# Kernel optimization log

Hardware: AMD Instinct MI355X
Metric: run time of the kernel (lower is better)

The kernel has to match this reference:

```python
import jax, jax.numpy as jnp
import numpy as np

N = 10000        # nodes
E = 320000       # edges (before self-loops)
G = 100          # graphs in batch
HEADS = 2
OUT = 125        # per-head out channels
NEG_SLOPE = 0.2  # PyG GATConv default leaky_relu slope


def setup_inputs() -> dict:
    key = jax.random.key(0)
    k = lambda i: jax.random.fold_in(key, i)
    rn = lambda i, shape, s=0.1: jax.random.normal(k(i), shape, jnp.float32) * s
    inp = {
        "x": jax.random.normal(k(0), (N, 336), jnp.float32),
        "edge_index": jax.random.randint(k(1), (2, E), 0, N, jnp.int32),
        "batch": jnp.sort(jax.random.randint(k(2), (N,), 0, G, jnp.int32)),
    }
    conv_in = [336, 250, 250, 250]
    for i, din in enumerate(conv_in, start=1):
        base = 10 * i
        inp[f"W{i}"] = rn(base, (din, HEADS * OUT))
        inp[f"asrc{i}"] = rn(base + 1, (HEADS, OUT))
        inp[f"adst{i}"] = rn(base + 2, (HEADS, OUT))
        inp[f"b{i}"] = jnp.zeros((HEADS * OUT,), jnp.float32)
    lin_dims = [(250, 200), (200, 100), (100, 100), (100, 29)]
    for i, (din, dout) in enumerate(lin_dims, start=1):
        inp[f"lw{i}"] = rn(100 + i, (din, dout))
        inp[f"lb{i}"] = jnp.zeros((dout,), jnp.float32)
    return inp


def gat_conv(x, src, dst, W, asrc, adst, b):
    # PyG GATConv (v1), concat heads, self-loops already in (src, dst).
    n = x.shape[0]
    h = (x @ W).reshape(n, HEADS, OUT)                    # [N,H,C]
    e_src = jnp.einsum('nhc,hc->nh', h, asrc)             # a_src . h_j
    e_dst = jnp.einsum('nhc,hc->nh', h, adst)             # a_dst . h_i
    e = jax.nn.leaky_relu(e_src[src] + e_dst[dst], NEG_SLOPE)  # [Etot,H]
    m = jax.ops.segment_max(e, dst, num_segments=n)       # segment softmax over incoming edges
    e = jnp.exp(e - m[dst])
    denom = jax.ops.segment_sum(e, dst, num_segments=n)
    alpha = e / (denom[dst] + 1e-16)                      # [Etot,H]
    out = jax.ops.segment_sum(alpha[:, :, None] * h[src], dst, num_segments=n)
    return out.reshape(n, HEADS * OUT) + b


def reference(x, edge_index, batch,
              W1, asrc1, adst1, b1, W2, asrc2, adst2, b2,
              W3, asrc3, adst3, b3, W4, asrc4, adst4, b4,
              lw1, lb1, lw2, lb2, lw3, lb3, lw4, lb4):
    n = x.shape[0]
    loop = jnp.arange(n, dtype=edge_index.dtype)
    src = jnp.concatenate([edge_index[0], loop])          # add_self_loops=True
    dst = jnp.concatenate([edge_index[1], loop])

    h = jax.nn.relu(gat_conv(x, src, dst, W1, asrc1, adst1, b1))
    h = jax.nn.relu(gat_conv(h, src, dst, W2, asrc2, adst2, b2))
    h = jax.nn.relu(gat_conv(h, src, dst, W3, asrc3, adst3, b3))
    h = jax.nn.relu(gat_conv(h, src, dst, W4, asrc4, adst4, b4))

    # global_mean_pool over graph ids
    sums = jax.ops.segment_sum(h, batch, num_segments=G)
    cnts = jax.ops.segment_sum(jnp.ones((n, 1), h.dtype), batch, num_segments=G)
    g = sums / jnp.maximum(cnts, 1.0)                     # [G,250]

    g = jax.nn.relu(g @ lw1 + lb1)
    g = jax.nn.relu(g @ lw2 + lb2)
    g = jax.nn.relu(g @ lw3 + lb3)
    return g @ lw4 + lb4                                  # [G,29]
```

## Files before the change

kernel.cpp:

```cpp
#include <hip/hip_runtime.h>
#include <hip/hip_bf16.h>

#define NNODES 10000
#define NEDGES 320000
#define ETOT   (NEDGES + NNODES)
#define NGRAPH 100
#define CH     250
#define HOUT   125
#define MPAD   10048
#define KP0    352
#define KP1    256
#define HPAD   256
#define DCAP   256

typedef __attribute__((ext_vector_type(8))) short bf16x8;
typedef __attribute__((ext_vector_type(4))) float f32x4;

static __device__ __forceinline__ float bfbits2f(unsigned int u){
  union{ unsigned int i; float f; } v; v.i = u << 16; return v.f;
}
static __device__ __forceinline__ unsigned short f2bfbits(float f){
  __hip_bfloat16 b = __float2bfloat16(f);
  union{ __hip_bfloat16 b; unsigned short s; } v; v.b = b; return v.s;
}

__global__ void k_deg(const int* __restrict__ eidx, int* __restrict__ deg,
                      const int* __restrict__ batch, int* __restrict__ gstart){
  int e = blockIdx.x*blockDim.x + threadIdx.x;
  if (e < ETOT){
    int dst = (e < NEDGES) ? eidx[NEDGES + e] : (e - NEDGES);
    atomicAdd(&deg[dst], 1);
  }
  if (e < NNODES){
    int b1 = batch[e];
    int b0 = (e == 0) ? -1 : batch[e-1];
    for (int b = b0 + 1; b <= b1; ++b) gstart[b] = e;
    if (e == NNODES - 1){
      for (int b = b1 + 1; b <= NGRAPH; ++b) gstart[b] = NNODES;
    }
  }
}

__global__ __launch_bounds__(1024) void k_scan(const int* __restrict__ deg, int* __restrict__ rowptr){
  const int CHUNK = 10;
  int tid = threadIdx.x;
  int base = tid * CHUNK;
  int sum = 0;
  #pragma unroll
  for (int u = 0; u < CHUNK; ++u){
    int i = base + u;
    sum += (i < NNODES) ? deg[i] : 0;
  }
  int lane = tid & 63, wv = tid >> 6;
  int v = sum;
  #pragma unroll
  for (int off = 1; off < 64; off <<= 1){
    int t = __shfl_up(v, off);
    if (lane >= off) v += t;
  }
  __shared__ int wtot[16];
  __shared__ int woff[16];
  if (lane == 63) wtot[wv] = v;
  __syncthreads();
  if (tid == 0){
    int acc = 0;
    #pragma unroll
    for (int w = 0; w < 16; ++w){ woff[w] = acc; acc += wtot[w]; }
  }
  __syncthreads();
  int run = woff[wv] + v - sum;
  #pragma unroll
  for (int u = 0; u < CHUNK; ++u){
    int i = base + u;
    if (i < NNODES){
      run += deg[i];
      rowptr[i+1] = run;
    }
  }
  if (tid == 0) rowptr[0] = 0;
}

__global__ void k_fill(const int* __restrict__ eidx, const int* __restrict__ rowptr,
                       int* __restrict__ cursor, int* __restrict__ csr_src){
  int e = blockIdx.x*blockDim.x + threadIdx.x;
  if (e >= ETOT) return;
  int dst, src;
  if (e < NEDGES){ src = eidx[e]; dst = eidx[NEDGES + e]; }
  else           { src = e - NEDGES; dst = src; }
  int pos = atomicAdd(&cursor[dst], 1);
  csr_src[rowptr[dst] + pos] = src;
}

__global__ void k_xconv(const float* __restrict__ x, __hip_bfloat16* __restrict__ Ab){
  int idx = blockIdx.x*blockDim.x + threadIdx.x;
  if (idx >= NNODES*336) return;
  int r = idx / 336, k = idx % 336;
  Ab[(size_t)r * KP0 + k] = __float2bfloat16(x[idx]);
}

__global__ void k_wconv_all(const float* __restrict__ W0, const float* __restrict__ W1,
                            const float* __restrict__ W2, const float* __restrict__ W3,
                            __hip_bfloat16* __restrict__ Wt0, __hip_bfloat16* __restrict__ Wt1,
                            __hip_bfloat16* __restrict__ Wt2, __hip_bfloat16* __restrict__ Wt3){
  const int T0 = 16 * KP0 * 16;
  const int T1 = 16 * KP1 * 16;
  int idx = blockIdx.x*blockDim.x + threadIdx.x;
  const float* W; __hip_bfloat16* Wt; int K, Kp, li;
  if (idx < T0)              { W = W0; Wt = Wt0; K = 336; Kp = KP0; li = idx; }
  else if (idx < T0 +   T1)  { W = W1; Wt = Wt1; K = CH;  Kp = KP1; li = idx - T0; }
  else if (idx < T0 + 2*T1)  { W = W2; Wt = Wt2; K = CH;  Kp = KP1; li = idx - T0 - T1; }
  else if (idx < T0 + 3*T1)  { W = W3; Wt = Wt3; K = CH;  Kp = KP1; li = idx - T0 - 2*T1; }
  else return;
  int KC = Kp >> 5;
  int nt = li / (Kp * 16);
  int rem = li % (Kp * 16);
  int k = rem / 16;
  int n = rem % 16;
  int col = nt * 16 + n;
  float v = (k < K && col < CH) ? W[(size_t)k * CH + col] : 0.f;
  Wt[(((size_t)nt * KC + (k >> 5)) * 16 + n) * 32 + (k & 31)] = __float2bfloat16(v);
}

__global__ __launch_bounds__(256) void k_gemm_mfma(
    const __hip_bfloat16* __restrict__ A, const __hip_bfloat16* __restrict__ Wt,
    __hip_bfloat16* __restrict__ Cb, const float* __restrict__ asrc,
    const float* __restrict__ adst, float* __restrict__ esrc, float* __restrict__ edst,
    int M, int Kp){
  int wv = threadIdx.x >> 6, lane = threadIdx.x & 63;
  int n16 = lane & 15, q = lane >> 4;
  int KC = Kp >> 5;
  int rowbase = blockIdx.x * 64 + wv * 16;
  int bn = blockIdx.y * 64;
  int nt0 = bn >> 4;
  const __hip_bfloat16* ap = A  + (size_t)(rowbase + n16) * Kp + q * 8;
  const __hip_bfloat16* bp = Wt + ((size_t)nt0 * KC * 16 + n16) * 32 + q * 8;
  f32x4 ac0 = {0.f,0.f,0.f,0.f}, ac1 = ac0, ac2 = ac0, ac3 = ac0;
  for (int kc = 0; kc < KC; ++kc){
    bf16x8 a  = *(const bf16x8*)(ap + (size_t)kc * 32);
    bf16x8 b0 = *(const bf16x8*)(bp + ((size_t)0 * KC + kc) * 512);
    bf16x8 b1 = *(const bf16x8*)(bp + ((size_t)1 * KC + kc) * 512);
    bf16x8 b2 = *(const bf16x8*)(bp + ((size_t)2 * KC + kc) * 512);
    bf16x8 b3 = *(const bf16x8*)(bp + ((size_t)3 * KC + kc) * 512);
    ac0 = __builtin_amdgcn_mfma_f32_16x16x32_bf16(a, b0, ac0, 0, 0, 0);
    ac1 = __builtin_amdgcn_mfma_f32_16x16x32_bf16(a, b1, ac1, 0, 0, 0);
    ac2 = __builtin_amdgcn_mfma_f32_16x16x32_bf16(a, b2, ac2, 0, 0, 0);
    ac3 = __builtin_amdgcn_mfma_f32_16x16x32_bf16(a, b3, ac3, 0, 0, 0);
  }
  float es0[4] = {}, es1[4] = {}, ed0a[4] = {}, ed1a[4] = {};
  #define SCORE_T(AC, T) { \
    int col = bn + (T)*16 + n16; \
    bool ok = col < CH; \
    float av = ok ? asrc[col] : 0.f; \
    float dv = ok ? adst[col] : 0.f; \
    bool hh = col >= HOUT; \
    float av0 = hh ? 0.f : av, av1 = hh ? av : 0.f; \
    float dv0 = hh ? 0.f : dv, dv1 = hh ? dv : 0.f; \
    _Pragma("unroll") \
    for (int r = 0; r < 4; ++r){ \
      es0[r] += AC[r]*av0; es1[r] += AC[r]*av1; \
      ed0a[r] += AC[r]*dv0; ed1a[r] += AC[r]*dv1; } }
  SCORE_T(ac0, 0) SCORE_T(ac1, 1) SCORE_T(ac2, 2) SCORE_T(ac3, 3)
  #undef SCORE_T
  #pragma unroll
  for (int off = 1; off < 16; off <<= 1){
    #pragma unroll
    for (int r = 0; r < 4; ++r){
      es0[r]  += __shfl_xor(es0[r],  off);
      es1[r]  += __shfl_xor(es1[r],  off);
      ed0a[r] += __shfl_xor(ed0a[r], off);
      ed1a[r] += __shfl_xor(ed1a[r], off);
    }
  }
  if (n16 == 0){
    #pragma unroll
    for (int r = 0; r < 4; ++r){
      int row = rowbase + q*4 + r;
      if (row < M){
        atomicAdd(&esrc[row*2+0], es0[r]);
        atomicAdd(&esrc[row*2+1], es1[r]);
        atomicAdd(&edst[row*2+0], ed0a[r]);
        atomicAdd(&edst[row*2+1], ed1a[r]);
      }
    }
  }
  #pragma unroll
  for (int r = 0; r < 4; ++r){
    int row = rowbase + q * 4 + r;
    if (row >= M) continue;
    int col = bn + n16;
    __hip_bfloat16* cb = Cb + (size_t)row * HPAD + col;
    if (col      < CH) cb[0]  = __float2bfloat16(ac0[r]);
    if (col + 16 < CH) cb[16] = __float2bfloat16(ac1[r]);
    if (col + 32 < CH) cb[32] = __float2bfloat16(ac2[r]);
    if (col + 48 < CH) cb[48] = __float2bfloat16(ac3[r]);
  }
}

__global__ __launch_bounds__(256) void k_attn(const __hip_bfloat16* __restrict__ h,
                        const float* __restrict__ esrc, const float* __restrict__ edst,
                        const int* __restrict__ rowptr, const int* __restrict__ csr_src,
                        const float* __restrict__ bias, __hip_bfloat16* __restrict__ outb,
                        float* __restrict__ esZ, float* __restrict__ edZ){
  int node = blockIdx.x;
  int tid = threadIdx.x, wave = tid >> 6, lane = tid & 63;
  int start = rowptr[node], deg = rowptr[node+1] - start;
  __shared__ int   s_src[DCAP];
  __shared__ float s_x0[DCAP], s_x1[DCAP];
  __shared__ float wred0[4], wred1[4];
  __shared__ float sh[4 * 256];
  float ed0 = edst[node*2+0], ed1 = edst[node*2+1];
  float sm0 = 0.f, sm1 = 0.f;
  for (int i = tid; i < deg; i += 256){
    int src = csr_src[start + i];
    float e0 = esrc[src*2+0] + ed0; e0 = e0 > 0.f ? e0 : 0.2f*e0;
    float e1 = esrc[src*2+1] + ed1; e1 = e1 > 0.f ? e1 : 0.2f*e1;
    float x0 = __expf(e0), x1 = __expf(e1);
    if (i < DCAP){ s_src[i] = src; s_x0[i] = x0; s_x1[i] = x1; }
    sm0 += x0; sm1 += x1;
  }
  for (int off = 32; off > 0; off >>= 1){
    sm0 += __shfl_xor(sm0, off);
    sm1 += __shfl_xor(sm1, off);
  }
  if (lane == 0){ wred0[wave] = sm0; wred1[wave] = sm1; }
  __syncthreads();
  float inv0 = 1.f / ((wred0[0]+wred0[1]+wred0[2]+wred0[3]) + 1e-16f);
  float inv1 = 1.f / ((wred1[0]+wred1[1]+wred1[2]+wred1[3]) + 1e-16f);
  int c0 = 4*lane;
  bool h0_0 = (c0    ) < HOUT, h0_1 = (c0 + 1) < HOUT;
  bool h0_2 = (c0 + 2) < HOUT, h0_3 = (c0 + 3) < HOUT;
  float acc0=0.f, acc1=0.f, acc2=0.f, acc3=0.f;
  #define FETCH(I, S, A0, A1) { \
    if ((I) < DCAP){ S = s_src[I]; A0 = s_x0[I]*inv0; A1 = s_x1[I]*inv1; } \
    else { S = csr_src[start + (I)]; \
      float e0 = esrc[S*2+0] + ed0; e0 = e0 > 0.f ? e0 : 0.2f*e0; \
      float e1 = esrc[S*2+1] + ed1; e1 = e1 > 0.f ? e1 : 0.2f*e1; \
      A0 = __expf(e0)*inv0; A1 = __expf(e1)*inv1; } }
  #define GATHER(S, A0, A1) { \
    uint2 d = *(const uint2*)(h + (size_t)(S) * HPAD + c0); \
    acc0 += (h0_0 ? A0 : A1) * bfbits2f(d.x & 0xffffu); \
    acc1 += (h0_1 ? A0 : A1) * bfbits2f(d.x >> 16); \
    acc2 += (h0_2 ? A0 : A1) * bfbits2f(d.y & 0xffffu); \
    acc3 += (h0_3 ? A0 : A1) * bfbits2f(d.y >> 16); }
  int i = wave;
  for (; i + 4 < deg; i += 8){
    int sA, sB; float a0A,a1A,a0B,a1B;
    FETCH(i, sA, a0A, a1A)
    FETCH(i+4, sB, a0B, a1B)
    GATHER(sA, a0A, a1A)
    GATHER(sB, a0B, a1B)
  }
  if (i < deg){
    int sA; float a0A, a1A;
    FETCH(i, sA, a0A, a1A)
    GATHER(sA, a0A, a1A)
  }
  #undef GATHER
  #undef FETCH
  float* shw = sh + wave * 256;
  *(float4*)&shw[c0] = make_float4(acc0, acc1, acc2, acc3);
  __syncthreads();
  if (tid < 62){
    int c = 4*tid;
    float4 b4 = *(const float4*)&bias[c];
    float v0 = sh[c]   + sh[256+c]   + sh[512+c]   + sh[768+c]   + b4.x;
    float v1 = sh[c+1] + sh[256+c+1] + sh[512+c+1] + sh[768+c+1] + b4.y;
    float v2 = sh[c+2] + sh[256+c+2] + sh[512+c+2] + sh[768+c+2] + b4.z;
    float v3 = sh[c+3] + sh[256+c+3] + sh[512+c+3] + sh[768+c+3] + b4.w;
    v0 = v0 > 0.f ? v0 : 0.f; v1 = v1 > 0.f ? v1 : 0.f;
    v2 = v2 > 0.f ? v2 : 0.f; v3 = v3 > 0.f ? v3 : 0.f;
    ushort4 o; o.x = f2bfbits(v0); o.y = f2bfbits(v1); o.z = f2bfbits(v2); o.w = f2bfbits(v3);
    *(ushort4*)(outb + (size_t)node * KP1 + c) = o;
  } else if (tid == 62){
    #pragma unroll
    for (int j = 0; j < 2; ++j){
      int c = 248 + j;
      float v = sh[c] + sh[256+c] + sh[512+c] + sh[768+c] + bias[c];
      v = v > 0.f ? v : 0.f;
      outb[(size_t)node * KP1 + c] = __float2bfloat16(v);
    }
  }
  if (tid < 2){
    esZ[node*2 + tid] = 0.f;
    edZ[node*2 + tid] = 0.f;
  }
}

__global__ __launch_bounds__(256) void k_head(const __hip_bfloat16* __restrict__ xb,
                        const int* __restrict__ gstart,
                        const float* __restrict__ lw1, const float* __restrict__ lb1,
                        const float* __restrict__ lw2, const float* __restrict__ lb2,
                        const float* __restrict__ lw3, const float* __restrict__ lb3,
                        const float* __restrict__ lw4, const float* __restrict__ lb4,
                        float* __restrict__ out){
  int g = blockIdx.x;
  int tid = threadIdx.x;
  int s = gstart[g], e = gstart[g+1];
  __shared__ float gvec[256];
  __shared__ float m1[200];
  __shared__ float m2[112];
  __shared__ float m3[112];
  if (tid < CH){
    float a0=0.f,a1=0.f,a2=0.f,a3=0.f;
    int n = s;
    for (; n + 3 < e; n += 4){
      a0 += __bfloat162float(xb[(size_t)n     * KP1 + tid]);
      a1 += __bfloat162float(xb[(size_t)(n+1) * KP1 + tid]);
      a2 += __bfloat162float(xb[(size_t)(n+2) * KP1 + tid]);
      a3 += __bfloat162float(xb[(size_t)(n+3) * KP1 + tid]);
    }
    for (; n < e; ++n) a0 += __bfloat162float(xb[(size_t)n * KP1 + tid]);
    float scale = 1.f / fmaxf((float)(e - s), 1.f);
    gvec[tid] = (a0 + a1 + a2 + a3) * scale;
  }
  __syncthreads();
  if (tid < 200){
    float a0=0.f,a1=0.f,a2=0.f,a3=0.f;
    int k = 0;
    for (; k + 3 < CH; k += 4){
      a0 += gvec[k]   * lw1[(size_t)k     * 200 + tid];
      a1 += gvec[k+1] * lw1[(size_t)(k+1) * 200 + tid];
      a2 += gvec[k+2] * lw1[(size_t)(k+2) * 200 + tid];
      a3 += gvec[k+3] * lw1[(size_t)(k+3) * 200 + tid];
    }
    for (; k < CH; ++k) a0 += gvec[k] * lw1[(size_t)k * 200 + tid];
    float v = a0 + a1 + a2 + a3 + lb1[tid];
    m1[tid] = v > 0.f ? v : 0.f;
  }
  __syncthreads();
  if (tid < 100){
    float a0=0.f,a1=0.f,a2=0.f,a3=0.f;
    for (int k = 0; k + 3 < 200; k += 4){
      a0 += m1[k]   * lw2[(size_t)k     * 100 + tid];
      a1 += m1[k+1] * lw2[(size_t)(k+1) * 100 + tid];
      a2 += m1[k+2] * lw2[(size_t)(k+2) * 100 + tid];
      a3 += m1[k+3] * lw2[(size_t)(k+3) * 100 + tid];
    }
    float v = a0 + a1 + a2 + a3 + lb2[tid];
    m2[tid] = v > 0.f ? v : 0.f;
  }
  __syncthreads();
  if (tid < 100){
    float a0=0.f,a1=0.f,a2=0.f,a3=0.f;
    for (int k = 0; k + 3 < 100; k += 4){
      a0 += m2[k]   * lw3[(size_t)k     * 100 + tid];
      a1 += m2[k+1] * lw3[(size_t)(k+1) * 100 + tid];
      a2 += m2[k+2] * lw3[(size_t)(k+2) * 100 + tid];
      a3 += m2[k+3] * lw3[(size_t)(k+3) * 100 + tid];
    }
    float v = a0 + a1 + a2 + a3 + lb3[tid];
    m3[tid] = v > 0.f ? v : 0.f;
  }
  __syncthreads();
  if (tid < 29){
    float a0=0.f,a1=0.f,a2=0.f,a3=0.f;
    for (int k = 0; k + 3 < 100; k += 4){
      a0 += m3[k]   * lw4[(size_t)k     * 29 + tid];
      a1 += m3[k+1] * lw4[(size_t)(k+1) * 29 + tid];
      a2 += m3[k+2] * lw4[(size_t)(k+2) * 29 + tid];
      a3 += m3[k+3] * lw4[(size_t)(k+3) * 29 + tid];
    }
    out[(size_t)g * 29 + tid] = a0 + a1 + a2 + a3 + lb4[tid];
  }
}

extern "C" void kernel_launch(void* const* d_in, const int* in_sizes, int n_in,
                              void* d_out, int out_size, void* d_ws, size_t ws_size,
                              hipStream_t stream){
  const float* x   = (const float*)d_in[0];
  const int* eidx  = (const int*)d_in[1];
  const int* batch = (const int*)d_in[2];

  char* ws = (char*)d_ws;
  size_t off = 0;
  auto alloc = [&](size_t bytes)->void*{
    void* p = ws + off;
    off = (off + bytes + 255) & ~(size_t)255;
    return p;
  };
  __hip_bfloat16* hb16 = (__hip_bfloat16*)alloc((size_t)NNODES * HPAD * 2);
  __hip_bfloat16* Abf0 = (__hip_bfloat16*)alloc((size_t)MPAD * KP0 * 2);
  __hip_bfloat16* Abf  = (__hip_bfloat16*)alloc((size_t)MPAD * KP1 * 2);
  __hip_bfloat16* Wt0  = (__hip_bfloat16*)alloc((size_t)16 * KP0 * 16 * 2);
  __hip_bfloat16* Wt1  = (__hip_bfloat16*)alloc((size_t)16 * KP1 * 16 * 2);
  __hip_bfloat16* Wt2  = (__hip_bfloat16*)alloc((size_t)16 * KP1 * 16 * 2);
  __hip_bfloat16* Wt3  = (__hip_bfloat16*)alloc((size_t)16 * KP1 * 16 * 2);
  size_t zbeg = off;
  int*   deg    = (int*)  alloc((size_t)NNODES * 4);
  int*   cursor = (int*)  alloc((size_t)NNODES * 4);
  float* esA  = (float*)alloc((size_t)NNODES * 2 * 4);
  float* edA  = (float*)alloc((size_t)NNODES * 2 * 4);
  float* esB  = (float*)alloc((size_t)NNODES * 2 * 4);
  float* edB  = (float*)alloc((size_t)NNODES * 2 * 4);
  size_t zend = off;
  int*    rowptr  = (int*)   alloc((size_t)(NNODES + 1) * 4);
  int*    csr_src = (int*)   alloc((size_t)ETOT * 4);
  int*    gstart  = (int*)   alloc((size_t)(NGRAPH + 1) * 4);

  hipMemsetAsync(ws + zbeg, 0, zend - zbeg, stream);

  k_deg <<<(ETOT + 255)/256, 256, 0, stream>>>(eidx, deg, batch, gstart);
  k_scan<<<1, 1024, 0, stream>>>(deg, rowptr);
  k_fill<<<(ETOT + 255)/256, 256, 0, stream>>>(eidx, rowptr, cursor, csr_src);

  k_xconv<<<(NNODES*336 + 255)/256, 256, 0, stream>>>(x, Abf0);
  {
    int wtot = 16*KP0*16 + 3*16*KP1*16;
    k_wconv_all<<<(wtot + 255)/256, 256, 0, stream>>>(
        (const float*)d_in[3], (const float*)d_in[7], (const float*)d_in[11], (const float*)d_in[15],
        Wt0, Wt1, Wt2, Wt3);
  }

  const __hip_bfloat16* Wts[4] = {Wt0, Wt1, Wt2, Wt3};
  for (int L = 0; L < 4; ++L){
    const float* as_ = (const float*)d_in[4 + 4*L];
    const float* ad_ = (const float*)d_in[5 + 4*L];
    const float* bb  = (const float*)d_in[6 + 4*L];
    int Kp = (L == 0) ? KP0 : KP1;
    const __hip_bfloat16* Ain = (L == 0) ? Abf0 : Abf;
    float* es  = (L & 1) ? esB : esA;
    float* ed  = (L & 1) ? edB : edA;
    float* esZ = (L & 1) ? esA : esB;
    float* edZ = (L & 1) ? edA : edB;

    dim3 gg(MPAD/64, 4);
    k_gemm_mfma<<<gg, 256, 0, stream>>>(Ain, Wts[L], hb16, as_, ad_, es, ed, NNODES, Kp);
    k_attn<<<NNODES, 256, 0, stream>>>(hb16, es, ed, rowptr, csr_src, bb, Abf, esZ, edZ);
  }

  const float* lw1 = (const float*)d_in[19];
  const float* lb1 = (const float*)d_in[20];
  const float* lw2 = (const float*)d_in[21];
  const float* lb2 = (const float*)d_in[22];
  const float* lw3 = (const float*)d_in[23];
  const float* lb3 = (const float*)d_in[24];
  const float* lw4 = (const float*)d_in[25];
  const float* lb4 = (const float*)d_in[26];

  k_head<<<NGRAPH, 256, 0, stream>>>(Abf, gstart, lw1, lb1, lw2, lb2, lw3, lb3,
                                     lw4, lb4, (float*)d_out);
}
```

Measured before the change: 365.4 us.

## Assign one wave per node in attention and fuse preprocessing kernels

The attention kernel now processes four nodes per 256-thread block, one wavefront per node. This removes the cross-wave shared-memory reduction and the block barriers per node. The degree, batch-start, x-conversion and weight-conversion kernels are merged into one grid-stride preprocessing kernel, and the scan now runs on a 256-thread block, which cuts launch count. The trade-off is that each node's edge loop is serialized within one wave, and the per-wave shared edge cache is halved to 128 entries, so high-degree nodes fall back to recomputing scores.

```diff
diff --git a/kernel.cpp b/kernel.cpp
--- a/kernel.cpp
+++ b/kernel.cpp
@@ -8,10 +8,11 @@
 #define CH     250
 #define HOUT   125
 #define MPAD   10048
+#define NTILE  157
 #define KP0    352
 #define KP1    256
 #define HPAD   256
-#define DCAP   256
+#define DCAPW  128
 
 typedef __attribute__((ext_vector_type(8))) short bf16x8;
 typedef __attribute__((ext_vector_type(4))) float f32x4;
@@ -24,25 +25,54 @@
   union{ __hip_bfloat16 b; unsigned short s; } v; v.b = b; return v.s;
 }
 
-__global__ void k_deg(const int* __restrict__ eidx, int* __restrict__ deg,
-                      const int* __restrict__ batch, int* __restrict__ gstart){
-  int e = blockIdx.x*blockDim.x + threadIdx.x;
-  if (e < ETOT){
-    int dst = (e < NEDGES) ? eidx[NEDGES + e] : (e - NEDGES);
-    atomicAdd(&deg[dst], 1);
-  }
-  if (e < NNODES){
-    int b1 = batch[e];
-    int b0 = (e == 0) ? -1 : batch[e-1];
-    for (int b = b0 + 1; b <= b1; ++b) gstart[b] = e;
-    if (e == NNODES - 1){
-      for (int b = b1 + 1; b <= NGRAPH; ++b) gstart[b] = NNODES;
-    }
-  }
-}
-
-__global__ __launch_bounds__(1024) void k_scan(const int* __restrict__ deg, int* __restrict__ rowptr){
-  const int CHUNK = 10;
+struct Args {
+  const float* x; const int* eidx; const int* batch;
+  const float *W0,*W1,*W2,*W3;
+  __hip_bfloat16 *hb16, *Abf0, *Abf, *Wt0, *Wt1, *Wt2, *Wt3;
+  int *deg, *cursor, *rowptr, *csr_src, *gstart;
+};
+
+__global__ void k_pre(Args a){
+  int gtid = blockIdx.x * blockDim.x + threadIdx.x;
+  int gstr = gridDim.x * blockDim.x;
+  for (int e = gtid; e < ETOT; e += gstr){
+    int dst = (e < NEDGES) ? a.eidx[NEDGES + e] : (e - NEDGES);
+    atomicAdd(&a.deg[dst], 1);
+  }
+  for (int n = gtid; n < NNODES; n += gstr){
+    int b1 = a.batch[n];
+    int b0 = (n == 0) ? -1 : a.batch[n-1];
+    for (int b = b0 + 1; b <= b1; ++b) a.gstart[b] = n;
+    if (n == NNODES - 1){
+      for (int b = b1 + 1; b <= NGRAPH; ++b) a.gstart[b] = NNODES;
+    }
+  }
+  for (int i = gtid; i < NNODES*336; i += gstr){
+    int r = i / 336, k = i % 336;
+    a.Abf0[(size_t)r * KP0 + k] = __float2bfloat16(a.x[i]);
+  }
+  const int T0 = 16 * KP0 * 16;
+  const int T1 = 16 * KP1 * 16;
+  int tot = T0 + 3*T1;
+  for (int i = gtid; i < tot; i += gstr){
+    const float* W; __hip_bfloat16* Wt; int K, Kp, li;
+    if (i < T0)             { W = a.W0; Wt = a.Wt0; K = 336; Kp = KP0; li = i; }
+    else if (i < T0 +   T1) { W = a.W1; Wt = a.Wt1; K = CH;  Kp = KP1; li = i - T0; }
+    else if (i < T0 + 2*T1) { W = a.W2; Wt = a.Wt2; K = CH;  Kp = KP1; li = i - T0 - T1; }
+    else                    { W = a.W3; Wt = a.Wt3; K = CH;  Kp = KP1; li = i - T0 - 2*T1; }
+    int KC = Kp >> 5;
+    int nt = li / (Kp * 16);
+    int rem = li % (Kp * 16);
+    int k = rem / 16;
+    int n = rem % 16;
+    int col = nt * 16 + n;
+    float v = (k < K && col < CH) ? W[(size_t)k * CH + col] : 0.f;
+    Wt[(((size_t)nt * KC + (k >> 5)) * 16 + n) * 32 + (k & 31)] = __float2bfloat16(v);
+  }
+}
+
+__global__ __launch_bounds__(256) void k_scan(const int* __restrict__ deg, int* __restrict__ rowptr){
+  const int CHUNK = 40;
   int tid = threadIdx.x;
   int base = tid * CHUNK;
   int sum = 0;
@@ -58,14 +88,14 @@
     int t = __shfl_up(v, off);
     if (lane >= off) v += t;
   }
-  __shared__ int wtot[16];
-  __shared__ int woff[16];
+  __shared__ int wtot[4];
+  __shared__ int woff[4];
   if (lane == 63) wtot[wv] = v;
   __syncthreads();
   if (tid == 0){
     int acc = 0;
     #pragma unroll
-    for (int w = 0; w < 16; ++w){ woff[w] = acc; acc += wtot[w]; }
+    for (int w = 0; w < 4; ++w){ woff[w] = acc; acc += wtot[w]; }
   }
   __syncthreads();
   int run = woff[wv] + v - sum;
@@ -80,52 +110,21 @@
   if (tid == 0) rowptr[0] = 0;
 }
 
-__global__ void k_fill(const int* __restrict__ eidx, const int* __restrict__ rowptr,
-                       int* __restrict__ cursor, int* __restrict__ csr_src){
-  int e = blockIdx.x*blockDim.x + threadIdx.x;
+__global__ void k_fill(Args a){
+  int e = blockIdx.x * blockDim.x + threadIdx.x;
   if (e >= ETOT) return;
   int dst, src;
-  if (e < NEDGES){ src = eidx[e]; dst = eidx[NEDGES + e]; }
+  if (e < NEDGES){ src = a.eidx[e]; dst = a.eidx[NEDGES + e]; }
   else           { src = e - NEDGES; dst = src; }
-  int pos = atomicAdd(&cursor[dst], 1);
-  csr_src[rowptr[dst] + pos] = src;
-}
-
-__global__ void k_xconv(const float* __restrict__ x, __hip_bfloat16* __restrict__ Ab){
-  int idx = blockIdx.x*blockDim.x + threadIdx.x;
-  if (idx >= NNODES*336) return;
-  int r = idx / 336, k = idx % 336;
-  Ab[(size_t)r * KP0 + k] = __float2bfloat16(x[idx]);
-}
-
-__global__ void k_wconv_all(const float* __restrict__ W0, const float* __restrict__ W1,
-                            const float* __restrict__ W2, const float* __restrict__ W3,
-                            __hip_bfloat16* __restrict__ Wt0, __hip_bfloat16* __restrict__ Wt1,
-                            __hip_bfloat16* __restrict__ Wt2, __hip_bfloat16* __restrict__ Wt3){
-  const int T0 = 16 * KP0 * 16;
-  const int T1 = 16 * KP1 * 16;
-  int idx = blockIdx.x*blockDim.x + threadIdx.x;
-  const float* W; __hip_bfloat16* Wt; int K, Kp, li;
-  if (idx < T0)              { W = W0; Wt = Wt0; K = 336; Kp = KP0; li = idx; }
-  else if (idx < T0 +   T1)  { W = W1; Wt = Wt1; K = CH;  Kp = KP1; li = idx - T0; }
-  else if (idx < T0 + 2*T1)  { W = W2; Wt = Wt2; K = CH;  Kp = KP1; li = idx - T0 - T1; }
-  else if (idx < T0 + 3*T1)  { W = W3; Wt = Wt3; K = CH;  Kp = KP1; li = idx - T0 - 2*T1; }
-  else return;
-  int KC = Kp >> 5;
-  int nt = li / (Kp * 16);
-  int rem = li % (Kp * 16);
-  int k = rem / 16;
-  int n = rem % 16;
-  int col = nt * 16 + n;
-  float v = (k < K && col < CH) ? W[(size_t)k * CH + col] : 0.f;
-  Wt[(((size_t)nt * KC + (k >> 5)) * 16 + n) * 32 + (k & 31)] = __float2bfloat16(v);
-}
-
-__global__ __launch_bounds__(256) void k_gemm_mfma(
+  int pos = atomicAdd(&a.cursor[dst], 1);
+  a.csr_src[a.rowptr[dst] + pos] = src;
+}
+
+__global__ __launch_bounds__(256) void k_gemm(
     const __hip_bfloat16* __restrict__ A, const __hip_bfloat16* __restrict__ Wt,
     __hip_bfloat16* __restrict__ Cb, const float* __restrict__ asrc,
     const float* __restrict__ adst, float* __restrict__ esrc, float* __restrict__ edst,
-    int M, int Kp){
+    int Kp){
   int wv = threadIdx.x >> 6, lane = threadIdx.x & 63;
   int n16 = lane & 15, q = lane >> 4;
   int KC = Kp >> 5;
@@ -175,7 +174,7 @@
     #pragma unroll
     for (int r = 0; r < 4; ++r){
       int row = rowbase + q*4 + r;
-      if (row < M){
+      if (row < NNODES){
         atomicAdd(&esrc[row*2+0], es0[r]);
         atomicAdd(&esrc[row*2+1], es1[r]);
         atomicAdd(&edst[row*2+0], ed0a[r]);
@@ -186,7 +185,7 @@
   #pragma unroll
   for (int r = 0; r < 4; ++r){
     int row = rowbase + q * 4 + r;
-    if (row >= M) continue;
+    if (row >= NNODES) continue;
     int col = bn + n16;
     __hip_bfloat16* cb = Cb + (size_t)row * HPAD + col;
     if (col      < CH) cb[0]  = __float2bfloat16(ac0[r]);
@@ -201,37 +200,35 @@
                         const int* __restrict__ rowptr, const int* __restrict__ csr_src,
                         const float* __restrict__ bias, __hip_bfloat16* __restrict__ outb,
                         float* __restrict__ esZ, float* __restrict__ edZ){
-  int node = blockIdx.x;
-  int tid = threadIdx.x, wave = tid >> 6, lane = tid & 63;
+  int wv = threadIdx.x >> 6, lane = threadIdx.x & 63;
+  int node = blockIdx.x * 4 + wv;
+  __shared__ int   s_src[4][DCAPW];
+  __shared__ float s_x0[4][DCAPW], s_x1[4][DCAPW];
   int start = rowptr[node], deg = rowptr[node+1] - start;
-  __shared__ int   s_src[DCAP];
-  __shared__ float s_x0[DCAP], s_x1[DCAP];
-  __shared__ float wred0[4], wred1[4];
-  __shared__ float sh[4 * 256];
   float ed0 = edst[node*2+0], ed1 = edst[node*2+1];
   float sm0 = 0.f, sm1 = 0.f;
-  for (int i = tid; i < deg; i += 256){
+  for (int i = lane; i < deg; i += 64){
     int src = csr_src[start + i];
     float e0 = esrc[src*2+0] + ed0; e0 = e0 > 0.f ? e0 : 0.2f*e0;
     float e1 = esrc[src*2+1] + ed1; e1 = e1 > 0.f ? e1 : 0.2f*e1;
     float x0 = __expf(e0), x1 = __expf(e1);
-    if (i < DCAP){ s_src[i] = src; s_x0[i] = x0; s_x1[i] = x1; }
+    if (i < DCAPW){ s_src[wv][i] = src; s_x0[wv][i] = x0; s_x1[wv][i] = x1; }
     sm0 += x0; sm1 += x1;
   }
+  #pragma unroll
   for (int off = 32; off > 0; off >>= 1){
     sm0 += __shfl_xor(sm0, off);
     sm1 += __shfl_xor(sm1, off);
   }
-  if (lane == 0){ wred0[wave] = sm0; wred1[wave] = sm1; }
-  __syncthreads();
-  float inv0 = 1.f / ((wred0[0]+wred0[1]+wred0[2]+wred0[3]) + 1e-16f);
-  float inv1 = 1.f / ((wred1[0]+wred1[1]+wred1[2]+wred1[3]) + 1e-16f);
+  float inv0 = 1.f / (sm0 + 1e-16f);
+  float inv1 = 1.f / (sm1 + 1e-16f);
+  __syncthreads();
   int c0 = 4*lane;
   bool h0_0 = (c0    ) < HOUT, h0_1 = (c0 + 1) < HOUT;
   bool h0_2 = (c0 + 2) < HOUT, h0_3 = (c0 + 3) < HOUT;
   float acc0=0.f, acc1=0.f, acc2=0.f, acc3=0.f;
   #define FETCH(I, S, A0, A1) { \
-    if ((I) < DCAP){ S = s_src[I]; A0 = s_x0[I]*inv0; A1 = s_x1[I]*inv1; } \
+    if ((I) < DCAPW){ S = s_src[wv][I]; A0 = s_x0[wv][I]*inv0; A1 = s_x1[wv][I]*inv1; } \
     else { S = csr_src[start + (I)]; \
       float e0 = esrc[S*2+0] + ed0; e0 = e0 > 0.f ? e0 : 0.2f*e0; \
       float e1 = esrc[S*2+1] + ed1; e1 = e1 > 0.f ? e1 : 0.2f*e1; \
@@ -242,11 +239,11 @@
     acc1 += (h0_1 ? A0 : A1) * bfbits2f(d.x >> 16); \
     acc2 += (h0_2 ? A0 : A1) * bfbits2f(d.y & 0xffffu); \
     acc3 += (h0_3 ? A0 : A1) * bfbits2f(d.y >> 16); }
-  int i = wave;
-  for (; i + 4 < deg; i += 8){
+  int i = 0;
+  for (; i + 1 < deg; i += 2){
     int sA, sB; float a0A,a1A,a0B,a1B;
     FETCH(i, sA, a0A, a1A)
-    FETCH(i+4, sB, a0B, a1B)
+    FETCH(i+1, sB, a0B, a1B)
     GATHER(sA, a0A, a1A)
     GATHER(sB, a0B, a1B)
   }
@@ -257,32 +254,23 @@
   }
   #undef GATHER
   #undef FETCH
-  float* shw = sh + wave * 256;
-  *(float4*)&shw[c0] = make_float4(acc0, acc1, acc2, acc3);
-  __syncthreads();
-  if (tid < 62){
-    int c = 4*tid;
-    float4 b4 = *(const float4*)&bias[c];
-    float v0 = sh[c]   + sh[256+c]   + sh[512+c]   + sh[768+c]   + b4.x;
-    float v1 = sh[c+1] + sh[256+c+1] + sh[512+c+1] + sh[768+c+1] + b4.y;
-    float v2 = sh[c+2] + sh[256+c+2] + sh[512+c+2] + sh[768+c+2] + b4.z;
-    float v3 = sh[c+3] + sh[256+c+3] + sh[512+c+3] + sh[768+c+3] + b4.w;
+  if (lane < 62){
+    float4 b4 = *(const float4*)&bias[c0];
+    float v0 = acc0 + b4.x, v1 = acc1 + b4.y, v2 = acc2 + b4.z, v3 = acc3 + b4.w;
     v0 = v0 > 0.f ? v0 : 0.f; v1 = v1 > 0.f ? v1 : 0.f;
     v2 = v2 > 0.f ? v2 : 0.f; v3 = v3 > 0.f ? v3 : 0.f;
     ushort4 o; o.x = f2bfbits(v0); o.y = f2bfbits(v1); o.z = f2bfbits(v2); o.w = f2bfbits(v3);
-    *(ushort4*)(outb + (size_t)node * KP1 + c) = o;
-  } else if (tid == 62){
-    #pragma unroll
-    for (int j = 0; j < 2; ++j){
-      int c = 248 + j;
-      float v = sh[c] + sh[256+c] + sh[512+c] + sh[768+c] + bias[c];
-      v = v > 0.f ? v : 0.f;
-      outb[(size_t)node * KP1 + c] = __float2bfloat16(v);
-    }
-  }
-  if (tid < 2){
-    esZ[node*2 + tid] = 0.f;
-    edZ[node*2 + tid] = 0.f;
+    *(ushort4*)(outb + (size_t)node * KP1 + c0) = o;
+  } else if (lane == 62){
+    float v0 = acc0 + bias[248];
+    float v1 = acc1 + bias[249];
+    v0 = v0 > 0.f ? v0 : 0.f; v1 = v1 > 0.f ? v1 : 0.f;
+    outb[(size_t)node * KP1 + 248] = __float2bfloat16(v0);
+    outb[(size_t)node * KP1 + 249] = __float2bfloat16(v1);
+  }
+  if (lane < 2){
+    esZ[node*2 + lane] = 0.f;
+    edZ[node*2 + lane] = 0.f;
   }
 }
 
@@ -367,10 +355,6 @@
 extern "C" void kernel_launch(void* const* d_in, const int* in_sizes, int n_in,
                               void* d_out, int out_size, void* d_ws, size_t ws_size,
                               hipStream_t stream){
-  const float* x   = (const float*)d_in[0];
-  const int* eidx  = (const int*)d_in[1];
-  const int* batch = (const int*)d_in[2];
-
   char* ws = (char*)d_ws;
   size_t off = 0;
   auto alloc = [&](size_t bytes)->void*{
@@ -393,23 +377,26 @@
   float* esB  = (float*)alloc((size_t)NNODES * 2 * 4);
   float* edB  = (float*)alloc((size_t)NNODES * 2 * 4);
   size_t zend = off;
-  int*    rowptr  = (int*)   alloc((size_t)(NNODES + 1) * 4);
-  int*    csr_src = (int*)   alloc((size_t)ETOT * 4);
-  int*    gstart  = (int*)   alloc((size_t)(NGRAPH + 1) * 4);
+  int*   rowptr  = (int*)alloc((size_t)(NNODES + 1) * 4);
+  int*   csr_src = (int*)alloc((size_t)ETOT * 4);
+  int*   gstart  = (int*)alloc((size_t)(NGRAPH + 1) * 4);
 
   hipMemsetAsync(ws + zbeg, 0, zend - zbeg, stream);
 
-  k_deg <<<(ETOT + 255)/256, 256, 0, stream>>>(eidx, deg, batch, gstart);
-  k_scan<<<1, 1024, 0, stream>>>(deg, rowptr);
-  k_fill<<<(ETOT + 255)/256, 256, 0, stream>>>(eidx, rowptr, cursor, csr_src);
-
-  k_xconv<<<(NNODES*336 + 255)/256, 256, 0, stream>>>(x, Abf0);
-  {
-    int wtot = 16*KP0*16 + 3*16*KP1*16;
-    k_wconv_all<<<(wtot + 255)/256, 256, 0, stream>>>(
-        (const float*)d_in[3], (const float*)d_in[7], (const float*)d_in[11], (const float*)d_in[15],
-        Wt0, Wt1, Wt2, Wt3);
-  }
+  Args a;
+  a.x = (const float*)d_in[0];
+  a.eidx = (const int*)d_in[1];
+  a.batch = (const int*)d_in[2];
+  a.W0 = (const float*)d_in[3];  a.W1 = (const float*)d_in[7];
+  a.W2 = (const float*)d_in[11]; a.W3 = (const float*)d_in[15];
+  a.hb16 = hb16; a.Abf0 = Abf0; a.Abf = Abf;
+  a.Wt0 = Wt0; a.Wt1 = Wt1; a.Wt2 = Wt2; a.Wt3 = Wt3;
+  a.deg = deg; a.cursor = cursor; a.rowptr = rowptr;
+  a.csr_src = csr_src; a.gstart = gstart;
+
+  k_pre <<<(ETOT + 255)/256, 256, 0, stream>>>(a);
+  k_scan<<<1, 256, 0, stream>>>(deg, rowptr);
+  k_fill<<<(ETOT + 255)/256, 256, 0, stream>>>(a);
 
   const __hip_bfloat16* Wts[4] = {Wt0, Wt1, Wt2, Wt3};
   for (int L = 0; L < 4; ++L){
@@ -423,20 +410,14 @@
     float* esZ = (L & 1) ? esA : esB;
     float* edZ = (L & 1) ? edA : edB;
 
-    dim3 gg(MPAD/64, 4);
-    k_gemm_mfma<<<gg, 256, 0, stream>>>(Ain, Wts[L], hb16, as_, ad_, es, ed, NNODES, Kp);
-    k_attn<<<NNODES, 256, 0, stream>>>(hb16, es, ed, rowptr, csr_src, bb, Abf, esZ, edZ);
-  }
-
-  const float* lw1 = (const float*)d_in[19];
-  const float* lb1 = (const float*)d_in[20];
-  const float* lw2 = (const float*)d_in[21];
-  const float* lb2 = (const float*)d_in[22];
-  const float* lw3 = (const float*)d_in[23];
-  const float* lb3 = (const float*)d_in[24];
-  const float* lw4 = (const float*)d_in[25];
-  const float* lb4 = (const float*)d_in[26];
-
-  k_head<<<NGRAPH, 256, 0, stream>>>(Abf, gstart, lw1, lb1, lw2, lb2, lw3, lb3,
-                                     lw4, lb4, (float*)d_out);
-}
+    k_gemm<<<dim3(NTILE, 4), 256, 0, stream>>>(Ain, Wts[L], hb16, as_, ad_, es, ed, Kp);
+    k_attn<<<NNODES/4, 256, 0, stream>>>(hb16, es, ed, rowptr, csr_src, bb, Abf, esZ, edZ);
+  }
+
+  k_head<<<NGRAPH, 256, 0, stream>>>(Abf, gstart,
+      (const float*)d_in[19], (const float*)d_in[20],
+      (const float*)d_in[21], (const float*)d_in[22],
+      (const float*)d_in[23], (const float*)d_in[24],
+      (const float*)d_in[25], (const float*)d_in[26],
+      (float*)d_out);
+}
```

After: 362.8 us. No clear change (-0.7%).
